# Kernel tuning notes

Hardware: AMD Instinct MI355X
Metric: run time of the kernel (lower is better)

Reference implementation:

```python
import jax, jax.numpy as jnp
import numpy as np
import math

R, C, E, H = 512, 512, 256, 8
D = E // H

def setup_inputs() -> dict:
    key = jax.random.key(0)
    ks = jax.random.split(key, 10)
    x = jax.random.normal(ks[0], (R, C, E), dtype=jnp.float32)
    mask = (jax.random.uniform(ks[1], (R, C)) < 0.1).astype(jnp.float32)
    s = 1.0 / math.sqrt(E)
    Wq = jax.random.normal(ks[2], (E, E), dtype=jnp.float32) * s
    Wk = jax.random.normal(ks[3], (E, E), dtype=jnp.float32) * s
    Wv = jax.random.normal(ks[4], (E, E), dtype=jnp.float32) * s
    Wo = jax.random.normal(ks[5], (E, E), dtype=jnp.float32) * s
    bq = jnp.zeros((E,), jnp.float32)
    bk = jnp.zeros((E,), jnp.float32)
    bv = jnp.zeros((E,), jnp.float32)
    bo = jnp.zeros((E,), jnp.float32)
    return {"x": x, "mask": mask, "Wq": Wq, "bq": bq, "Wk": Wk, "bk": bk,
            "Wv": Wv, "bv": bv, "Wo": Wo, "bo": bo}

def reference(x, mask, Wq, bq, Wk, bk, Wv, bv, Wo, bo):
    r, c, e = x.shape
    scaling = (D ** -0.5) / math.sqrt(r)  # align_scaling
    # projections -> [R, C, H, D]
    q = (x @ Wq + bq).reshape(r, c, H, D)
    k = (x @ Wk + bk).reshape(r, c, H, D)
    q = q * scaling
    q = q * (1.0 - mask[:, :, None, None])  # zero padded query positions
    # shared row-summed attention logits: sum over rows r -> [H, C, C]
    attn_weights = jnp.einsum('rihd,rjhd->hij', q, k)
    m0 = mask[0][None, :, None]  # [1, C, 1] broadcast over heads and j
    attn_weights = attn_weights * (1.0 - m0) + m0 * (-10000.0)
    attn_probs = jax.nn.softmax(attn_weights, axis=-1)  # [H, C, C]
    # dropout rate is 0 -> identity
    v = (x @ Wv + bv).reshape(r, c, H, D)
    context = jnp.einsum('hij,rjhd->rihd', attn_probs, v).reshape(r, c, e)
    output = context @ Wo + bo
    return (output, attn_probs)
```

## Files before the change

kernel.cpp:

```cpp
#include <hip/hip_runtime.h>
#include <math.h>

#define R_ 512
#define C_ 512
#define E_ 256
#define H_ 8
#define D_ 32
#define RC_ (R_*C_)
#define RP 136

typedef __attribute__((ext_vector_type(8))) short bf16x8;
typedef __attribute__((ext_vector_type(4))) float f32x4;

__device__ __forceinline__ ushort f2bf(float f) {
    union { float f; unsigned u; } v; v.f = f;
    unsigned r = v.u + 0x7FFFu + ((v.u >> 16) & 1u);
    return (ushort)(r >> 16);
}
__device__ __forceinline__ float bf2f(ushort u) {
    union { unsigned u; float f; } v; v.u = ((unsigned)u) << 16;
    return v.f;
}

__device__ __forceinline__ void gll16(const ushort* g, ushort* l) {
#if __has_builtin(__builtin_amdgcn_global_load_lds)
    __builtin_amdgcn_global_load_lds(
        (const __attribute__((address_space(1))) unsigned*)(unsigned long long)g,
        (__attribute__((address_space(3))) unsigned*)(unsigned)(unsigned long long)l,
        16, 0, 0);
#else
    *(uint4*)l = *(const uint4*)g;
#endif
}

#define SCH(gbase, stride, lds, f)                                               \
    gll16((gbase) + (size_t)((f) >> 2) * (stride)                                \
              + (((((f) & 3) ^ ((((f) >> 2) >> 1) & 3))) << 3),                  \
          (lds) + (f) * 8)

#define SCHED0   __builtin_amdgcn_sched_barrier(0)
#define ABAR     __builtin_amdgcn_s_barrier()
#define VMCNT(N) asm volatile("s_waitcnt vmcnt(" #N ")" ::: "memory")
#define LGKM0    asm volatile("s_waitcnt lgkmcnt(0)" ::: "memory")
#define SYNC_IN(N) do { VMCNT(N); SCHED0; ABAR; SCHED0; } while (0)
#define SYNC_OUT   do { LGKM0; SCHED0; ABAR; SCHED0; } while (0)

#define PREAMBLE(WM, WN)                                \
    const int t = threadIdx.x;                          \
    const int wid = t >> 6, l = t & 63;                 \
    const int wm = (WM), wn = (WN);                     \
    const int l15 = l & 15, lhi = l >> 4;               \
    const int swz8 = (lhi ^ ((l15 >> 1) & 3)) * 8;      \
    f32x4 acc[4][4];                                    \
    _Pragma("unroll")                                   \
    for (int a_ = 0; a_ < 4; ++a_)                      \
        _Pragma("unroll")                               \
        for (int b_ = 0; b_ < 4; ++b_)                  \
            acc[a_][b_] = (f32x4){0.f, 0.f, 0.f, 0.f};

#define MFMA_STEP(As, Bs)                                                        \
    {                                                                            \
        bf16x8 af_[4], bf_[4];                                                   \
        _Pragma("unroll")                                                        \
        for (int f_ = 0; f_ < 4; ++f_) {                                         \
            af_[f_] = *(const bf16x8*)((As) + (wm*64 + f_*16 + l15)*32 + swz8);  \
            bf_[f_] = *(const bf16x8*)((Bs) + (wn*64 + f_*16 + l15)*32 + swz8);  \
        }                                                                        \
        _Pragma("unroll")                                                        \
        for (int m_ = 0; m_ < 4; ++m_)                                           \
            _Pragma("unroll")                                                    \
            for (int n_ = 0; n_ < 4; ++n_)                                       \
                acc[m_][n_] = __builtin_amdgcn_mfma_f32_16x16x32_bf16(           \
                    af_[m_], bf_[n_], acc[m_][n_], 0, 0, 0);                     \
    }

#define DBUFC(STG, NIT)                                                          \
    STG(0, A0, B0);                                                              \
    for (int itp = 0; itp < (NIT)/2; ++itp) {                                    \
        STG(2*itp+1, A1, B1);                                                    \
        SYNC_IN(4);                                                              \
        MFMA_STEP(A0, B0);                                                       \
        SYNC_OUT;                                                                \
        if (itp < (NIT)/2 - 1) { STG(2*itp+2, A0, B0); SYNC_IN(4); }             \
        else                   { SYNC_IN(0); }                                   \
        MFMA_STEP(A1, B1);                                                       \
        SYNC_OUT;                                                                \
    }

__global__ __launch_bounds__(256) void convert_x(
    const float* __restrict__ x, ushort* __restrict__ xb)
{
    const size_t blk = (size_t)blockIdx.x * 4096;
    #pragma unroll
    for (int c = 0; c < 4; ++c) {
        const size_t s = blk + ((size_t)threadIdx.x + 256 * c) * 4;
        float4 a = *(const float4*)(x + s);
        ushort o[4] = {f2bf(a.x), f2bf(a.y), f2bf(a.z), f2bf(a.w)};
        *(uint2*)(xb + s) = *(uint2*)o;
    }
}

__global__ __launch_bounds__(256) void convert_w(
    const float* __restrict__ Wq, const float* __restrict__ Wk,
    const float* __restrict__ Wv, const float* __restrict__ Wo,
    ushort* __restrict__ WTqkv, ushort* __restrict__ WoT)
{
    const int id = blockIdx.x;
    const int matn = id >> 8;
    const int n = id & 255;
    const int k = threadIdx.x;
    const float* W = (matn == 0) ? Wq : (matn == 1) ? Wk : (matn == 2) ? Wv : Wo;
    ushort v = f2bf(W[(size_t)k * E_ + n]);
    if (matn < 3) WTqkv[((size_t)matn * E_ + n) * E_ + k] = v;
    else          WoT[(size_t)n * E_ + k] = v;
}

__global__ __launch_bounds__(256) void qkv_mfma(
    const ushort* __restrict__ xb, const ushort* __restrict__ WT,
    const float* __restrict__ bq, const float* __restrict__ bk,
    const float* __restrict__ bv, const float* __restrict__ mask,
    ushort* __restrict__ qb, ushort* __restrict__ kb, ushort* __restrict__ vb)
{
    __shared__ __align__(16) ushort S[128 * RP];
    ushort* A0 = S;
    ushort* B0 = S + 4096;
    ushort* A1 = S + 8192;
    ushort* B1 = S + 12288;
    const int id = ((blockIdx.x & 7) * 1536) + (blockIdx.x >> 3);
    const int nt = id % 6;
    const int rc0 = (id / 6) * 128;
    PREAMBLE(wid >> 1, wid & 1);

    const ushort* Ab = xb + (size_t)rc0 * E_;
    const ushort* Bb = WT + (size_t)nt * 128 * E_;

#define QSTG(i, Abuf, Bbuf) {                                   \
    const ushort* Ai = Ab + (i) * 32;                           \
    const ushort* Bi = Bb + (i) * 32;                           \
    SCH(Ai, E_, Abuf, t); SCH(Ai, E_, Abuf, t + 256);           \
    SCH(Bi, E_, Bbuf, t); SCH(Bi, E_, Bbuf, t + 256); }
    DBUFC(QSTG, 8);

    const int proj = nt >> 1;
    const float* bias = (proj == 0) ? bq : (proj == 1) ? bk : bv;
    float bvv[4];
    #pragma unroll
    for (int fn = 0; fn < 4; ++fn)
        bvv[fn] = bias[(nt * 128 + wn * 64 + fn * 16 + l15) & 255];

    #pragma unroll
    for (int fm = 0; fm < 4; ++fm)
        #pragma unroll
        for (int fn = 0; fn < 4; ++fn)
            #pragma unroll
            for (int rg = 0; rg < 4; ++rg) {
                const int m = wm * 64 + fm * 16 + lhi * 4 + rg;
                const int n = wn * 64 + fn * 16 + l15;
                const ushort val = f2bf(acc[fm][fn][rg] + bvv[fn]);
                if (proj < 2) S[m * RP + n] = val;
                else          S[n * RP + m] = val;
            }
    __syncthreads();

    const int r = rc0 >> 9, c0 = rc0 & 511;
    if (proj < 2) {
        ushort* dst = (proj == 0) ? qb : kb;
        #pragma unroll
        for (int c = 0; c < 8; ++c) {
            const int idx = t + 256 * c;
            const int mrow = idx >> 4, ne = (idx & 15) * 8;
            uint4 w = *(const uint4*)(S + mrow * RP + ne);
            if (proj == 0) {
                const float sk = 0.0078125f * (1.0f - mask[rc0 + mrow]);
                ushort* ws = (ushort*)&w;
                #pragma unroll
                for (int jj = 0; jj < 8; ++jj) ws[jj] = f2bf(bf2f(ws[jj]) * sk);
            }
            const int e = (nt & 1) * 128 + ne, h = e >> 5, d = e & 31;
            *(uint4*)(dst + ((((size_t)h * R_ + r) * C_) + c0 + mrow) * D_ + d) = w;
        }
    } else {
        #pragma unroll
        for (int c = 0; c < 8; ++c) {
            const int idx = t + 256 * c;
            const int nrow = idx >> 4, m0 = (idx & 15) * 8;
            uint4 w = *(const uint4*)(S + nrow * RP + m0);
            const int e = (nt & 1) * 128 + nrow, h = e >> 5, d = e & 31;
            *(uint4*)(vb + (((size_t)h * R_ + r) * D_ + d) * C_ + c0 + m0) = w;
        }
    }
}

__global__ __launch_bounds__(256) void logits_mfma(
    const ushort* __restrict__ qb, const ushort* __restrict__ kb,
    float* __restrict__ partial)
{
    __shared__ __align__(16) ushort S[16384];
    ushort* A0 = S;
    ushort* B0 = S + 4096;
    ushort* A1 = S + 8192;
    ushort* B1 = S + 12288;
    const int id = ((blockIdx.x & 7) * 128) + (blockIdx.x >> 3);
    const int sub = id & 15;
    const int j0 = (sub & 3) * 128;
    const int i0 = (sub >> 2) * 128;
    const int hks = id >> 4;
    const int h = hks >> 3, ks = hks & 7;
    PREAMBLE(wid >> 1, wid & 1);

    const ushort* Ab = qb + (((size_t)h * R_ + ks * 64) * C_ + i0) * D_;
    const ushort* Bb = kb + (((size_t)h * R_ + ks * 64) * C_ + j0) * D_;

#define LSTG(i, Abuf, Bbuf) {                                   \
    const ushort* Ai = Ab + (size_t)(i) * (C_ * D_);            \
    const ushort* Bi = Bb + (size_t)(i) * (C_ * D_);            \
    SCH(Ai, D_, Abuf, t); SCH(Ai, D_, Abuf, t + 256);           \
    SCH(Bi, D_, Bbuf, t); SCH(Bi, D_, Bbuf, t + 256); }
    DBUFC(LSTG, 64);

    float* dst = partial + ((size_t)ks * H_ + h) * C_ * C_;
    #pragma unroll
    for (int fm = 0; fm < 4; ++fm)
        #pragma unroll
        for (int rg = 0; rg < 4; ++rg) {
            const int i = i0 + wm * 64 + fm * 16 + lhi * 4 + rg;
            #pragma unroll
            for (int fn = 0; fn < 4; ++fn) {
                const int j = j0 + wn * 64 + fn * 16 + l15;
                dst[(size_t)i * C_ + j] = acc[fm][fn][rg];
            }
        }
}

__global__ __launch_bounds__(256) void softmax_kernel(
    const float* __restrict__ partial, const float* __restrict__ mask,
    float* __restrict__ probs, ushort* __restrict__ Pb)
{
    const int hi = blockIdx.x;
    const int i = hi & 511;
    const int t = threadIdx.x;
    const size_t base = (size_t)hi * C_;
    const size_t stride = (size_t)H_ * C_ * C_;
    float v0 = 0.f, v1 = 0.f;
    #pragma unroll
    for (int ksp = 0; ksp < 8; ++ksp) {
        v0 += partial[ksp * stride + base + t];
        v1 += partial[ksp * stride + base + t + 256];
    }
    const float mi = mask[i];
    const float keep = 1.0f - mi;
    v0 = v0 * keep + mi * (-10000.0f);
    v1 = v1 * keep + mi * (-10000.0f);

    float m = fmaxf(v0, v1);
    #pragma unroll
    for (int off = 32; off > 0; off >>= 1) m = fmaxf(m, __shfl_xor(m, off));
    __shared__ float red[4];
    if ((t & 63) == 0) red[t >> 6] = m;
    __syncthreads();
    m = fmaxf(fmaxf(red[0], red[1]), fmaxf(red[2], red[3]));

    const float e0 = expf(v0 - m), e1 = expf(v1 - m);
    float s = e0 + e1;
    #pragma unroll
    for (int off = 32; off > 0; off >>= 1) s += __shfl_xor(s, off);
    __syncthreads();
    if ((t & 63) == 0) red[t >> 6] = s;
    __syncthreads();
    s = red[0] + red[1] + red[2] + red[3];

    const float inv = 1.0f / s;
    const float p0 = e0 * inv, p1 = e1 * inv;
    probs[base + t] = p0;
    probs[base + t + 256] = p1;
    Pb[base + t] = f2bf(p0);
    Pb[base + t + 256] = f2bf(p1);
}

__global__ __launch_bounds__(256) void context_mfma(
    const ushort* __restrict__ Pb, const ushort* __restrict__ vb,
    ushort* __restrict__ ctxb)
{
    __shared__ __align__(16) ushort S[128 * RP];
    ushort* A0 = S;
    ushort* B0 = S + 4096;
    ushort* A1 = S + 8192;
    ushort* B1 = S + 12288;
    const int id = ((blockIdx.x & 7) * 512) + (blockIdx.x >> 3);
    const int i0 = (id & 3) * 128;
    const int n0 = ((id >> 2) & 127) * 128;
    const int h = id >> 9;
    PREAMBLE(wid >> 1, wid & 1);

    const ushort* Ab = Pb + ((size_t)h * C_ + i0) * C_;
    const ushort* Bb = vb + ((size_t)h * R_ * D_ + n0) * C_;

#define CSTG(i, Abuf, Bbuf) {                                   \
    const ushort* Ai = Ab + (i) * 32;                           \
    const ushort* Bi = Bb + (i) * 32;                           \
    SCH(Ai, C_, Abuf, t); SCH(Ai, C_, Abuf, t + 256);           \
    SCH(Bi, C_, Bbuf, t); SCH(Bi, C_, Bbuf, t + 256); }
    DBUFC(CSTG, 16);

    #pragma unroll
    for (int fm = 0; fm < 4; ++fm)
        #pragma unroll
        for (int fn = 0; fn < 4; ++fn)
            #pragma unroll
            for (int rg = 0; rg < 4; ++rg) {
                const int m = wm * 64 + fm * 16 + lhi * 4 + rg;
                const int n = wn * 64 + fn * 16 + l15;
                S[m * RP + n] = f2bf(acc[fm][fn][rg]);
            }
    __syncthreads();

    #pragma unroll
    for (int c = 0; c < 8; ++c) {
        const int idx = t + 256 * c;
        const int mrow = idx >> 4, nl = (idx & 15) * 8;
        uint4 w = *(const uint4*)(S + mrow * RP + nl);
        const int n = n0 + nl;
        const int rr = n >> 5, d = n & 31;
        const size_t rc = (size_t)rr * C_ + i0 + mrow;
        *(uint4*)(ctxb + rc * E_ + h * D_ + d) = w;
    }
}

__global__ __launch_bounds__(256) void out_proj_mfma(
    const ushort* __restrict__ ctxb, const ushort* __restrict__ WoT,
    const float* __restrict__ bo, float* __restrict__ out)
{
    __shared__ __align__(16) ushort S[128 * RP];
    ushort* A0 = S;
    ushort* B0 = S + 4096;
    ushort* A1 = S + 8192;
    ushort* B1 = S + 12288;
    float* Sf = (float*)S;
    const int id = ((blockIdx.x & 7) * 512) + (blockIdx.x >> 3);
    const int n0 = (id & 1) * 128;
    const int rc0 = (id >> 1) * 128;
    PREAMBLE(wid >> 1, wid & 1);

    const ushort* Ab = ctxb + (size_t)rc0 * E_;
    const ushort* Bb = WoT + (size_t)n0 * E_;

#define OSTG(i, Abuf, Bbuf) {                                   \
    const ushort* Ai = Ab + (i) * 32;                           \
    const ushort* Bi = Bb + (i) * 32;                           \
    SCH(Ai, E_, Abuf, t); SCH(Ai, E_, Abuf, t + 256);           \
    SCH(Bi, E_, Bbuf, t); SCH(Bi, E_, Bbuf, t + 256); }
    DBUFC(OSTG, 8);

    float bvv[4];
    #pragma unroll
    for (int fn = 0; fn < 4; ++fn)
        bvv[fn] = bo[n0 + wn * 64 + fn * 16 + l15];

    #pragma unroll
    for (int p = 0; p < 2; ++p) {
        #pragma unroll
        for (int fm = 0; fm < 4; ++fm)
            #pragma unroll
            for (int fh = 0; fh < 2; ++fh) {
                const int fn = 2 * p + fh;
                #pragma unroll
                for (int rg = 0; rg < 4; ++rg) {
                    const int m = wm * 64 + fm * 16 + lhi * 4 + rg;
                    const int s = wn * 32 + fh * 16 + l15;
                    Sf[m * 68 + s] = acc[fm][fn][rg] + bvv[fn];
                }
            }
        __syncthreads();
        #pragma unroll
        for (int c = 0; c < 8; ++c) {
            const int idx = t + 256 * c;
            const int row = idx >> 4, s0 = (idx & 15) * 4;
            float4 w = *(const float4*)(Sf + row * 68 + s0);
            const int ncol = n0 + (s0 >> 5) * 64 + (2 * p + ((s0 >> 4) & 1)) * 16 + (s0 & 15);
            *(float4*)(out + ((size_t)rc0 + row) * E_ + ncol) = w;
        }
        __syncthreads();
    }
}

extern "C" void kernel_launch(void* const* d_in, const int* in_sizes, int n_in,
                              void* d_out, int out_size, void* d_ws, size_t ws_size,
                              hipStream_t stream)
{
    const float* x    = (const float*)d_in[0];
    const float* mask = (const float*)d_in[1];
    const float* Wq   = (const float*)d_in[2];
    const float* bq   = (const float*)d_in[3];
    const float* Wk   = (const float*)d_in[4];
    const float* bk   = (const float*)d_in[5];
    const float* Wv   = (const float*)d_in[6];
    const float* bv   = (const float*)d_in[7];
    const float* Wo   = (const float*)d_in[8];
    const float* bo   = (const float*)d_in[9];

    float* out   = (float*)d_out;
    float* probs = out + (size_t)RC_ * E_;

    char* ws = (char*)d_ws;
    ushort* qb      = (ushort*)(ws);
    ushort* kb      = (ushort*)(ws + 134217728ull);
    ushort* vb      = (ushort*)(ws + 268435456ull);
    ushort* ctxb    = (ushort*)(ws + 402653184ull);
    float*  partial = (float*)(ws + 536870912ull);
    ushort* Pb      = (ushort*)(ws + 603979776ull);
    ushort* WTqkv   = (ushort*)(ws + 608174080ull);
    ushort* WoT     = (ushort*)(ws + 608567296ull);
    ushort* xb      = (ushort*)(ws + 608700416ull);

    convert_x<<<16384, 256, 0, stream>>>(x, xb);
    convert_w<<<1024, 256, 0, stream>>>(Wq, Wk, Wv, Wo, WTqkv, WoT);
    qkv_mfma<<<12288, 256, 0, stream>>>(xb, WTqkv, bq, bk, bv, mask, qb, kb, vb);
    logits_mfma<<<1024, 256, 0, stream>>>(qb, kb, partial);
    softmax_kernel<<<4096, 256, 0, stream>>>(partial, mask, probs, Pb);
    context_mfma<<<4096, 256, 0, stream>>>(Pb, vb, ctxb);
    out_proj_mfma<<<4096, 256, 0, stream>>>(ctxb, WoT, bo, out);
}
```

Measured before the change: 661.6 us.

## Switch GEMM main loops to triple-buffered LDS pipeline with one barrier per step

Replaces the double-buffered load/compute loop in all four MFMA GEMM kernels with a three-stage ring of LDS buffers. Global-to-LDS copies run two steps ahead, and each step needs only one barrier instead of two. The goal is to hide more memory latency and cut synchronisation overhead. In exchange, LDS per block grows to 48 KB, which may lower occupancy, and the loops are fully unrolled, which raises code size.

New measurement: 626.9 us. -5.3%, faster.

```diff
diff --git a/kernel.cpp b/kernel.cpp
--- a/kernel.cpp
+++ b/kernel.cpp
@@ -41,9 +41,6 @@
 #define SCHED0   __builtin_amdgcn_sched_barrier(0)
 #define ABAR     __builtin_amdgcn_s_barrier()
 #define VMCNT(N) asm volatile("s_waitcnt vmcnt(" #N ")" ::: "memory")
-#define LGKM0    asm volatile("s_waitcnt lgkmcnt(0)" ::: "memory")
-#define SYNC_IN(N) do { VMCNT(N); SCHED0; ABAR; SCHED0; } while (0)
-#define SYNC_OUT   do { LGKM0; SCHED0; ABAR; SCHED0; } while (0)
 
 #define PREAMBLE(WM, WN)                                \
     const int t = threadIdx.x;                          \
@@ -74,18 +71,25 @@
                     af_[m_], bf_[n_], acc[m_][n_], 0, 0, 0);                     \
     }
 
-#define DBUFC(STG, NIT)                                                          \
-    STG(0, A0, B0);                                                              \
-    for (int itp = 0; itp < (NIT)/2; ++itp) {                                    \
-        STG(2*itp+1, A1, B1);                                                    \
-        SYNC_IN(4);                                                              \
-        MFMA_STEP(A0, B0);                                                       \
-        SYNC_OUT;                                                                \
-        if (itp < (NIT)/2 - 1) { STG(2*itp+2, A0, B0); SYNC_IN(4); }             \
-        else                   { SYNC_IN(0); }                                   \
-        MFMA_STEP(A1, B1);                                                       \
-        SYNC_OUT;                                                                \
-    }
+#define DBUFT(STG, NIT)                                                          \
+    STG(0, A0, B0); STG(1, A1, B1);                                              \
+    _Pragma("unroll")                                                            \
+    for (int s = 0; s < (NIT); ++s) {                                            \
+        if (s < (NIT) - 1) { VMCNT(4); } else { VMCNT(0); }                      \
+        SCHED0; ABAR; SCHED0;                                                    \
+        if (s + 2 < (NIT)) {                                                     \
+            if (((s + 2) % 3) == 0)      { STG(s + 2, A0, B0); }                 \
+            else if (((s + 2) % 3) == 1) { STG(s + 2, A1, B1); }                 \
+            else                         { STG(s + 2, A2, B2); }                 \
+        }                                                                        \
+        if ((s % 3) == 0)      { MFMA_STEP(A0, B0); }                            \
+        else if ((s % 3) == 1) { MFMA_STEP(A1, B1); }                            \
+        else                   { MFMA_STEP(A2, B2); }                            \
+    }
+
+#define BUFS3 ushort* A0 = S;          ushort* B0 = S + 4096;                    \
+              ushort* A1 = S + 8192;   ushort* B1 = S + 12288;                   \
+              ushort* A2 = S + 16384;  ushort* B2 = S + 20480;
 
 __global__ __launch_bounds__(256) void convert_x(
     const float* __restrict__ x, ushort* __restrict__ xb)
@@ -121,11 +125,8 @@
     const float* __restrict__ bv, const float* __restrict__ mask,
     ushort* __restrict__ qb, ushort* __restrict__ kb, ushort* __restrict__ vb)
 {
-    __shared__ __align__(16) ushort S[128 * RP];
-    ushort* A0 = S;
-    ushort* B0 = S + 4096;
-    ushort* A1 = S + 8192;
-    ushort* B1 = S + 12288;
+    __shared__ __align__(16) ushort S[24576];
+    BUFS3;
     const int id = ((blockIdx.x & 7) * 1536) + (blockIdx.x >> 3);
     const int nt = id % 6;
     const int rc0 = (id / 6) * 128;
@@ -139,7 +140,8 @@
     const ushort* Bi = Bb + (i) * 32;                           \
     SCH(Ai, E_, Abuf, t); SCH(Ai, E_, Abuf, t + 256);           \
     SCH(Bi, E_, Bbuf, t); SCH(Bi, E_, Bbuf, t + 256); }
-    DBUFC(QSTG, 8);
+    DBUFT(QSTG, 8);
+    __syncthreads();
 
     const int proj = nt >> 1;
     const float* bias = (proj == 0) ? bq : (proj == 1) ? bk : bv;
@@ -195,11 +197,8 @@
     const ushort* __restrict__ qb, const ushort* __restrict__ kb,
     float* __restrict__ partial)
 {
-    __shared__ __align__(16) ushort S[16384];
-    ushort* A0 = S;
-    ushort* B0 = S + 4096;
-    ushort* A1 = S + 8192;
-    ushort* B1 = S + 12288;
+    __shared__ __align__(16) ushort S[24576];
+    BUFS3;
     const int id = ((blockIdx.x & 7) * 128) + (blockIdx.x >> 3);
     const int sub = id & 15;
     const int j0 = (sub & 3) * 128;
@@ -216,7 +215,7 @@
     const ushort* Bi = Bb + (size_t)(i) * (C_ * D_);            \
     SCH(Ai, D_, Abuf, t); SCH(Ai, D_, Abuf, t + 256);           \
     SCH(Bi, D_, Bbuf, t); SCH(Bi, D_, Bbuf, t + 256); }
-    DBUFC(LSTG, 64);
+    DBUFT(LSTG, 64);
 
     float* dst = partial + ((size_t)ks * H_ + h) * C_ * C_;
     #pragma unroll
@@ -281,11 +280,8 @@
     const ushort* __restrict__ Pb, const ushort* __restrict__ vb,
     ushort* __restrict__ ctxb)
 {
-    __shared__ __align__(16) ushort S[128 * RP];
-    ushort* A0 = S;
-    ushort* B0 = S + 4096;
-    ushort* A1 = S + 8192;
-    ushort* B1 = S + 12288;
+    __shared__ __align__(16) ushort S[24576];
+    BUFS3;
     const int id = ((blockIdx.x & 7) * 512) + (blockIdx.x >> 3);
     const int i0 = (id & 3) * 128;
     const int n0 = ((id >> 2) & 127) * 128;
@@ -300,7 +296,8 @@
     const ushort* Bi = Bb + (i) * 32;                           \
     SCH(Ai, C_, Abuf, t); SCH(Ai, C_, Abuf, t + 256);           \
     SCH(Bi, C_, Bbuf, t); SCH(Bi, C_, Bbuf, t + 256); }
-    DBUFC(CSTG, 16);
+    DBUFT(CSTG, 16);
+    __syncthreads();
 
     #pragma unroll
     for (int fm = 0; fm < 4; ++fm)
@@ -330,11 +327,8 @@
     const ushort* __restrict__ ctxb, const ushort* __restrict__ WoT,
     const float* __restrict__ bo, float* __restrict__ out)
 {
-    __shared__ __align__(16) ushort S[128 * RP];
-    ushort* A0 = S;
-    ushort* B0 = S + 4096;
-    ushort* A1 = S + 8192;
-    ushort* B1 = S + 12288;
+    __shared__ __align__(16) ushort S[24576];
+    BUFS3;
     float* Sf = (float*)S;
     const int id = ((blockIdx.x & 7) * 512) + (blockIdx.x >> 3);
     const int n0 = (id & 1) * 128;
@@ -349,7 +343,8 @@
     const ushort* Bi = Bb + (i) * 32;                           \
     SCH(Ai, E_, Abuf, t); SCH(Ai, E_, Abuf, t + 256);           \
     SCH(Bi, E_, Bbuf, t); SCH(Bi, E_, Bbuf, t + 256); }
-    DBUFC(OSTG, 8);
+    DBUFT(OSTG, 8);
+    __syncthreads();
 
     float bvv[4];
     #pragma unroll
```
